# Performance work log

Hardware: AMD Instinct MI355X
Metric: run time of the kernel (lower is better)

The kernel has to match this reference:

```python
import jax, jax.numpy as jnp
import numpy as np

N = 100000   # nodes
E = 3200000  # edges (avg degree 32)
NFEAT = 512
NHID = 8     # forced == 8 by (x_left + x_right) broadcast in the source
NCLASS = 16


def setup_inputs() -> dict:
    key = jax.random.key(0)
    ks = jax.random.split(key, 10)
    x = jax.random.normal(ks[0], (N, NFEAT), dtype=jnp.float32)
    adj_rows = jax.random.randint(ks[1], (E,), 0, N, dtype=jnp.int32)
    adj_cols = jax.random.randint(ks[2], (E,), 0, N, dtype=jnp.int32)
    adj_vals = jax.random.uniform(ks[3], (E,), dtype=jnp.float32)
    s1 = 1.0 / np.sqrt(NFEAT)
    s2 = 1.0 / np.sqrt(NHID)
    W1 = jax.random.normal(ks[4], (NFEAT, NHID), dtype=jnp.float32) * s1
    b1 = jnp.zeros((NHID,), dtype=jnp.float32)
    W2 = jax.random.normal(ks[5], (NHID, NCLASS), dtype=jnp.float32) * s2
    b2 = jnp.zeros((NCLASS,), dtype=jnp.float32)
    V = jax.random.normal(ks[6], (NFEAT, NHID), dtype=jnp.float32) * s1
    gamma = jnp.ones((NHID,), dtype=jnp.float32)
    beta = jnp.zeros((NHID,), dtype=jnp.float32)
    return {"x": x, "adj_rows": adj_rows, "adj_cols": adj_cols, "adj_vals": adj_vals,
            "W1": W1, "b1": b1, "W2": W2, "b2": b2, "V": V, "gamma": gamma, "beta": beta}


def reference(x, adj_rows, adj_cols, adj_vals, W1, b1, W2, b2, V, gamma, beta):
    n = x.shape[0]

    def spmm(support):  # adj @ support, adj in COO
        gathered = adj_vals[:, None] * support[adj_cols]        # [E, F]
        return jax.ops.segment_sum(gathered, adj_rows, num_segments=n)

    # gc1: relu(spmm(adj, x @ W1) + b1)   (dropout off: eval mode)
    x_left = jax.nn.relu(spmm(x @ W1) + b1)                     # [N, 8]

    # BI_Intereaction: FM bi-interaction pooling 0.5*((xV)^2 - (x^2)(V^2))
    xv = x @ V                                                  # [N, 8]
    x2v2 = (x * x) @ (V * V)                                    # [N, 8]
    x_right = jax.nn.relu(0.5 * (xv * xv - x2v2))

    # BatchNorm1d eval mode: running_mean=0, running_var=1 -> affine only
    x_right = gamma * x_right + beta

    h = 0.5 * (x_left + x_right)                                # [N, 8]
    out = spmm(h @ W2) + b2                                     # [N, 16]
    return jax.nn.log_softmax(out, axis=1)
```

## Files before the change

### kernel.cpp

```cpp
#include <hip/hip_runtime.h>
#include <cstdint>
#include <cstddef>


#define NFEAT 512
#define NHID 8
#define NCLASS 16
#define RPB 64
#define NB 512
#define BCAP 2368
#define NBINS_MAX 2048

#define DB_NODES 64
#define DB_CHUNK 32
#define DB_PAD 33
#define DB_BUF (DB_NODES * DB_PAD)

__device__ __forceinline__ void dense_body2(
    int node0, int tid,
    const float* __restrict__ x,
    const float* __restrict__ W1T, const float* __restrict__ VT,
    const float* __restrict__ VSQT,
    const float* __restrict__ gamma, const float* __restrict__ beta,
    float* __restrict__ xw1, float* __restrict__ right, int n_nodes,
    float* xs)
{
    const int lane = tid & 63;

    const int j0 = __builtin_amdgcn_readfirstlane(tid >> 6);
    const float* __restrict__ w1a = W1T  + j0 * NFEAT;
    const float* __restrict__ w1b = W1T  + (j0 + 4) * NFEAT;
    const float* __restrict__ va  = VT   + j0 * NFEAT;
    const float* __restrict__ vb  = VT   + (j0 + 4) * NFEAT;
    const float* __restrict__ sa  = VSQT + j0 * NFEAT;
    const float* __restrict__ sb  = VSQT + (j0 + 4) * NFEAT;

    const int row0 = tid >> 3, row1 = row0 + 32;
    const int col  = tid & 7;
    int gr0 = node0 + row0; if (gr0 >= n_nodes) gr0 = n_nodes - 1;
    int gr1 = node0 + row1; if (gr1 >= n_nodes) gr1 = n_nodes - 1;
    const float4* __restrict__ p0 = (const float4*)(x + (size_t)gr0 * NFEAT) + col;
    const float4* __restrict__ p1 = (const float4*)(x + (size_t)gr1 * NFEAT) + col;
    const int b0 = row0 * DB_PAD + col * 4;
    const int b1 = row1 * DB_PAD + col * 4;

    float a1a = 0.f, a1b = 0.f;
    float ava = 0.f, avb = 0.f;
    float a2a = 0.f, a2b = 0.f;
    const int xbase = lane * DB_PAD;

    {
        float4 c0 = p0[0], c1 = p1[0];
        xs[b0] = c0.x; xs[b0 + 1] = c0.y; xs[b0 + 2] = c0.z; xs[b0 + 3] = c0.w;
        xs[b1] = c1.x; xs[b1 + 1] = c1.y; xs[b1 + 2] = c1.z; xs[b1 + 3] = c1.w;
    }
    __syncthreads();

    for (int ch = 0; ch < NFEAT / DB_CHUNK; ++ch) {
        float4 n0, n1;
        const bool more = (ch + 1) < (NFEAT / DB_CHUNK);
        if (more) { n0 = p0[(ch + 1) * 8]; n1 = p1[(ch + 1) * 8]; }

        const float* xb = xs + (ch & 1) * DB_BUF + xbase;
        const int kof = ch * DB_CHUNK;
#pragma unroll
        for (int kk = 0; kk < DB_CHUNK / 4; ++kk) {
            const int kb = kof + kk * 4;
            float x0 = xb[kk * 4 + 0];
            float x1 = xb[kk * 4 + 1];
            float x2 = xb[kk * 4 + 2];
            float x3 = xb[kk * 4 + 3];
            float q0 = x0 * x0, q1 = x1 * x1, q2 = x2 * x2, q3 = x3 * x3;

            a1a += x0 * w1a[kb] + x1 * w1a[kb + 1] + x2 * w1a[kb + 2] + x3 * w1a[kb + 3];
            a1b += x0 * w1b[kb] + x1 * w1b[kb + 1] + x2 * w1b[kb + 2] + x3 * w1b[kb + 3];
            ava += x0 * va[kb]  + x1 * va[kb + 1]  + x2 * va[kb + 2]  + x3 * va[kb + 3];
            avb += x0 * vb[kb]  + x1 * vb[kb + 1]  + x2 * vb[kb + 2]  + x3 * vb[kb + 3];
            a2a += q0 * sa[kb]  + q1 * sa[kb + 1]  + q2 * sa[kb + 2]  + q3 * sa[kb + 3];
            a2b += q0 * sb[kb]  + q1 * sb[kb + 1]  + q2 * sb[kb + 2]  + q3 * sb[kb + 3];
        }

        if (more) {
            float* d = xs + ((ch + 1) & 1) * DB_BUF;
            d[b0] = n0.x; d[b0 + 1] = n0.y; d[b0 + 2] = n0.z; d[b0 + 3] = n0.w;
            d[b1] = n1.x; d[b1 + 1] = n1.y; d[b1 + 2] = n1.z; d[b1 + 3] = n1.w;
        }
        __syncthreads();
    }

    int node = node0 + lane;
    if (node < n_nodes) {
        float g0 = gamma[j0], g1 = gamma[j0 + 4];
        float b0_ = beta[j0], b1_ = beta[j0 + 4];
        xw1[node * 8 + j0]     = a1a;
        xw1[node * 8 + j0 + 4] = a1b;
        float ra = fmaxf(0.5f * (ava * ava - a2a), 0.f);
        float rb = fmaxf(0.5f * (avb * avb - a2b), 0.f);
        right[node * 8 + j0]     = 0.5f * (g0 * ra + b0_);
        right[node * 8 + j0 + 4] = 0.5f * (g1 * rb + b1_);
    }
}

__global__ __launch_bounds__(256) void dense_kernel(
    const float* __restrict__ x,
    const float* __restrict__ W1T, const float* __restrict__ VT,
    const float* __restrict__ VSQT,
    const float* __restrict__ gamma, const float* __restrict__ beta,
    float* __restrict__ xw1, float* __restrict__ right, int n_nodes)
{
    __shared__ float xs[2 * DB_BUF];
    dense_body2(blockIdx.x * DB_NODES, threadIdx.x, x, W1T, VT, VSQT,
                gamma, beta, xw1, right, n_nodes, xs);
}

__global__ __launch_bounds__(256) void prep_kernel(
    const float* __restrict__ W1, const float* __restrict__ V,
    float* __restrict__ W1T, float* __restrict__ VT, float* __restrict__ VSQT,
    uint4* __restrict__ zero_base, int zero_count16)
{
    int tid = blockIdx.x * 256 + threadIdx.x;
    if (tid < NFEAT * NHID) {
        int k = tid >> 3, j = tid & 7;
        W1T[j * NFEAT + k] = W1[tid];
        float vv = V[tid];
        VT[j * NFEAT + k] = vv;
        VSQT[j * NFEAT + k] = vv * vv;
    }
    int stride = gridDim.x * 256;
    for (int i = tid; i < zero_count16; i += stride)
        zero_base[i] = make_uint4(0u, 0u, 0u, 0u);
}

__global__ __launch_bounds__(256) void count_denseA_kernel(
    const int* __restrict__ rows, int* __restrict__ hist,
    int chunk, int nbins, int e,
    const float* __restrict__ x, const float* __restrict__ W1T,
    const float* __restrict__ VT, const float* __restrict__ VSQT,
    const float* __restrict__ gamma, const float* __restrict__ beta,
    float* __restrict__ xw1, float* __restrict__ right,
    int n_nodes, int dblocksA)
{
    __shared__ float xs[2 * DB_BUF];
    const int bid = blockIdx.x;
    const int tid = threadIdx.x;

    if (bid < dblocksA) {
        dense_body2(bid * DB_NODES, tid, x, W1T, VT, VSQT,
                    gamma, beta, xw1, right, n_nodes, xs);
        return;
    }

    const int cb = bid - dblocksA;
    int* histl = (int*)xs;
    for (int i = tid; i < nbins; i += 256) histl[i] = 0;
    __syncthreads();

    const int base = cb * chunk;
    int lim = e - base; if (lim > chunk) lim = chunk; if (lim < 0) lim = 0;
    const int nq = lim >> 2;
    for (int q = tid; q < nq; q += 256) {
        int4 r4 = *(const int4*)(rows + base + q * 4);
        atomicAdd(&histl[r4.x >> 6], 1);
        atomicAdd(&histl[r4.y >> 6], 1);
        atomicAdd(&histl[r4.z >> 6], 1);
        atomicAdd(&histl[r4.w >> 6], 1);
    }
    const int rem = lim & 3;
    if (tid < rem) atomicAdd(&histl[rows[base + nq * 4 + tid] >> 6], 1);
    __syncthreads();
    for (int i = tid; i < nbins; i += 256)
        hist[(size_t)i * NB + cb] = histl[i];
}

__global__ __launch_bounds__(NB) void scan_kernel(
    const int* __restrict__ hist, int* __restrict__ off,
    int* __restrict__ bintotal)
{
    __shared__ int sa[NB], sb[NB];
    const int bin = blockIdx.x;
    const int tid = threadIdx.x;
    const size_t base = (size_t)bin * NB;

    int h0 = hist[base + tid];
    sa[tid] = h0;
    __syncthreads();
    int* s = sa; int* d = sb;
    for (int o = 1; o < NB; o <<= 1) {
        d[tid] = s[tid] + (tid >= o ? s[tid - o] : 0);
        __syncthreads();
        int* t = s; s = d; d = t;
    }
    off[base + tid] = s[tid] - h0;
    if (tid == NB - 1) bintotal[bin] = s[NB - 1];
}

__global__ __launch_bounds__(256) void place_denseB_kernel(
    const int* __restrict__ rows, const int* __restrict__ cols,
    const float* __restrict__ vals, const int* __restrict__ off,
    unsigned long long* __restrict__ binbuf,
    int chunk, int nbins, int e,
    const float* __restrict__ x, const float* __restrict__ W1T,
    const float* __restrict__ VT, const float* __restrict__ VSQT,
    const float* __restrict__ gamma, const float* __restrict__ beta,
    float* __restrict__ xw1, float* __restrict__ right,
    int n_nodes, int dblocksB, int nodeB0)
{
    __shared__ float xs[2 * DB_BUF];
    const int bid = blockIdx.x;
    const int tid = threadIdx.x;

    if (bid < dblocksB) {
        dense_body2(nodeB0 + bid * DB_NODES, tid, x, W1T, VT, VSQT,
                    gamma, beta, xw1, right, n_nodes, xs);
        return;
    }

    const int cb = bid - dblocksB;
    int* cur = (int*)xs;
    for (int i = tid; i < nbins; i += 256)
        cur[i] = off[(size_t)i * NB + cb];
    __syncthreads();

    const int base = cb * chunk;
    int lim = e - base; if (lim > chunk) lim = chunk; if (lim < 0) lim = 0;
    const int nq = lim >> 2;
    for (int q = tid; q < nq; q += 256) {
        int i = base + q * 4;
        int4   r4 = *(const int4*)(rows + i);
        int4   c4 = *(const int4*)(cols + i);
        float4 v4 = *(const float4*)(vals + i);
#pragma unroll
        for (int u = 0; u < 4; ++u) {
            int r = (&r4.x)[u], c = (&c4.x)[u];
            float v = (&v4.x)[u];
            int bin = r >> 6;
            int slot = atomicAdd(&cur[bin], 1);
            if (slot < BCAP) {
                unsigned long long ev =
                    ((unsigned long long)__float_as_uint(v) << 32) |
                    ((unsigned)(r & (RPB - 1)) << 17) | (unsigned)(unsigned int)c;
                binbuf[(size_t)bin * BCAP + slot] = ev;
            }
        }
    }
    const int rem = lim & 3;
    if (tid < rem) {
        int i = base + nq * 4 + tid;
        int r = rows[i];
        int bin = r >> 6;
        int slot = atomicAdd(&cur[bin], 1);
        if (slot < BCAP) {
            unsigned long long ev =
                ((unsigned long long)__float_as_uint(vals[i]) << 32) |
                ((unsigned)(r & (RPB - 1)) << 17) | (unsigned)(unsigned int)cols[i];
            binbuf[(size_t)bin * BCAP + slot] = ev;
        }
    }
}

__global__ __launch_bounds__(512) void binspmm0_kernel(
    const unsigned long long* __restrict__ binbuf,
    const int* __restrict__ bintotal,
    unsigned long long* __restrict__ sortbuf,
    int* __restrict__ rowstart, int* __restrict__ rowcnt,
    const float* __restrict__ src,
    const float* __restrict__ b1, const float* __restrict__ right,
    float* __restrict__ dst, int n)
{
    __shared__ unsigned long long sorted[BCAP];
    __shared__ int hcnt[RPB];
    __shared__ int hstart[RPB];
    __shared__ int hcur[RPB];
    const int bin = blockIdx.x;
    const int tid = threadIdx.x;

    if (tid < RPB) hcnt[tid] = 0;
    __syncthreads();

    int total = bintotal[bin];
    if (total > BCAP) total = BCAP;
    const unsigned long long* bb = binbuf + (size_t)bin * BCAP;

    const int s0 = tid, s1 = tid + 512, s2 = tid + 1024, s3 = tid + 1536, s4 = tid + 2048;
    unsigned long long e0 = 0, e1 = 0, e2 = 0, e3 = 0, e4 = 0;
    if (s0 < total) { e0 = bb[s0]; atomicAdd(&hcnt[(int)((e0 >> 17) & (RPB - 1))], 1); }
    if (s1 < total) { e1 = bb[s1]; atomicAdd(&hcnt[(int)((e1 >> 17) & (RPB - 1))], 1); }
    if (s2 < total) { e2 = bb[s2]; atomicAdd(&hcnt[(int)((e2 >> 17) & (RPB - 1))], 1); }
    if (s3 < total) { e3 = bb[s3]; atomicAdd(&hcnt[(int)((e3 >> 17) & (RPB - 1))], 1); }
    if (s4 < total) { e4 = bb[s4]; atomicAdd(&hcnt[(int)((e4 >> 17) & (RPB - 1))], 1); }
    __syncthreads();

    if (tid < RPB) hstart[tid] = hcnt[tid];
    __syncthreads();
    for (int o = 1; o < RPB; o <<= 1) {
        int t = 0;
        if (tid < RPB) t = hstart[tid] + (tid >= o ? hstart[tid - o] : 0);
        __syncthreads();
        if (tid < RPB) hstart[tid] = t;
        __syncthreads();
    }
    if (tid < RPB) {
        int ex = hstart[tid] - hcnt[tid];
        hstart[tid] = ex;
        hcur[tid] = ex;
    }
    __syncthreads();

    if (s0 < total) { int rl = (int)((e0 >> 17) & (RPB - 1)); sorted[atomicAdd(&hcur[rl], 1)] = e0; }
    if (s1 < total) { int rl = (int)((e1 >> 17) & (RPB - 1)); sorted[atomicAdd(&hcur[rl], 1)] = e1; }
    if (s2 < total) { int rl = (int)((e2 >> 17) & (RPB - 1)); sorted[atomicAdd(&hcur[rl], 1)] = e2; }
    if (s3 < total) { int rl = (int)((e3 >> 17) & (RPB - 1)); sorted[atomicAdd(&hcur[rl], 1)] = e3; }
    if (s4 < total) { int rl = (int)((e4 >> 17) & (RPB - 1)); sorted[atomicAdd(&hcur[rl], 1)] = e4; }
    __syncthreads();

    for (int s = tid; s < total; s += 512)
        sortbuf[(size_t)bin * BCAP + s] = sorted[s];
    if (tid < RPB) {
        rowstart[bin * RPB + tid] = hstart[tid];
        rowcnt[bin * RPB + tid]   = hcnt[tid];
    }

    const int rl = tid >> 3, l = tid & 7;
    const int st = hstart[rl], cn = hcnt[rl];
    float a0 = 0.f, a1 = 0.f, a2 = 0.f, a3 = 0.f;
    float a4 = 0.f, a5 = 0.f, a6 = 0.f, a7 = 0.f;
    for (int i = st + l; i < st + cn; i += 8) {
        unsigned long long ev = sorted[i];
        int col = (int)(ev & 0x1FFFFu);
        float v = __uint_as_float((unsigned)(ev >> 32));
        const float4* sp = (const float4*)(src + (size_t)col * 8);
        float4 lo = sp[0], hi = sp[1];
        a0 += v * lo.x; a1 += v * lo.y; a2 += v * lo.z; a3 += v * lo.w;
        a4 += v * hi.x; a5 += v * hi.y; a6 += v * hi.z; a7 += v * hi.w;
    }
#pragma unroll
    for (int o2 = 1; o2 < 8; o2 <<= 1) {
        a0 += __shfl_xor(a0, o2); a1 += __shfl_xor(a1, o2);
        a2 += __shfl_xor(a2, o2); a3 += __shfl_xor(a3, o2);
        a4 += __shfl_xor(a4, o2); a5 += __shfl_xor(a5, o2);
        a6 += __shfl_xor(a6, o2); a7 += __shfl_xor(a7, o2);
    }

    const int g = bin * RPB + rl;
    if (g >= n) return;

    float s = l < 4 ? (l < 2 ? (l == 0 ? a0 : a1) : (l == 2 ? a2 : a3))
                    : (l < 6 ? (l == 4 ? a4 : a5) : (l == 6 ? a6 : a7));
    float hv = 0.5f * fmaxf(s + b1[l], 0.f) + right[(size_t)g * 8 + l];
    dst[(size_t)g * 8 + l] = hv;
}

__global__ __launch_bounds__(256) void walk1_kernel(
    const unsigned long long* __restrict__ sortbuf,
    const int* __restrict__ rowstart, const int* __restrict__ rowcnt,
    const float* __restrict__ src,
    const float* __restrict__ W2, const float* __restrict__ b2,
    float* __restrict__ out, int n)
{
    const int bin = blockIdx.x;
    const int tid = threadIdx.x;
    const int rl = tid >> 2, l = tid & 3;

    const int st = rowstart[bin * RPB + rl];
    const int cn = rowcnt[bin * RPB + rl];
    const unsigned long long* bb = sortbuf + (size_t)bin * BCAP;

    float a0 = 0.f, a1 = 0.f, a2 = 0.f, a3 = 0.f;
    float a4 = 0.f, a5 = 0.f, a6 = 0.f, a7 = 0.f;
    for (int i = st + l; i < st + cn; i += 4) {
        unsigned long long ev = bb[i];
        int col = (int)(ev & 0x1FFFFu);
        float v = __uint_as_float((unsigned)(ev >> 32));
        const float4* sp = (const float4*)(src + (size_t)col * 8);
        float4 lo = sp[0], hi = sp[1];
        a0 += v * lo.x; a1 += v * lo.y; a2 += v * lo.z; a3 += v * lo.w;
        a4 += v * hi.x; a5 += v * hi.y; a6 += v * hi.z; a7 += v * hi.w;
    }
#pragma unroll
    for (int o2 = 1; o2 < 4; o2 <<= 1) {
        a0 += __shfl_xor(a0, o2); a1 += __shfl_xor(a1, o2);
        a2 += __shfl_xor(a2, o2); a3 += __shfl_xor(a3, o2);
        a4 += __shfl_xor(a4, o2); a5 += __shfl_xor(a5, o2);
        a6 += __shfl_xor(a6, o2); a7 += __shfl_xor(a7, o2);
    }

    const int g = bin * RPB + rl;
    if (g >= n) return;

    float hv[NHID] = {a0, a1, a2, a3, a4, a5, a6, a7};
    float z[NCLASS];
#pragma unroll
    for (int cc = 0; cc < NCLASS; ++cc) z[cc] = b2[cc];
#pragma unroll
    for (int j = 0; j < NHID; ++j) {
#pragma unroll
        for (int cc = 0; cc < NCLASS; ++cc)
            z[cc] += hv[j] * W2[j * NCLASS + cc];
    }
    float m = z[0];
#pragma unroll
    for (int cc = 1; cc < NCLASS; ++cc) m = fmaxf(m, z[cc]);
    float s = 0.f;
#pragma unroll
    for (int cc = 0; cc < NCLASS; ++cc) s += __expf(z[cc] - m);
    float lse = m + __logf(s);
    float o0, o1, o2, o3;
    if (l == 0)      { o0 = z[0];  o1 = z[1];  o2 = z[2];  o3 = z[3];  }
    else if (l == 1) { o0 = z[4];  o1 = z[5];  o2 = z[6];  o3 = z[7];  }
    else if (l == 2) { o0 = z[8];  o1 = z[9];  o2 = z[10]; o3 = z[11]; }
    else             { o0 = z[12]; o1 = z[13]; o2 = z[14]; o3 = z[15]; }
    *(float4*)(out + (size_t)g * NCLASS + 4 * l) =
        make_float4(o0 - lse, o1 - lse, o2 - lse, o3 - lse);
}

__global__ __launch_bounds__(256) void spmm8_kernel(
    const int* __restrict__ rows, const int* __restrict__ cols,
    const float* __restrict__ vals, const float* __restrict__ src,
    float* __restrict__ acc, int n_edges)
{
    int tid = blockIdx.x * 256 + threadIdx.x;
    int e = tid >> 1;
    if (e >= n_edges) return;
    int hh = tid & 1;
    int r = rows[e], c = cols[e];
    float v = vals[e];
    float4 f = ((const float4*)src)[c * 2 + hh];
    float* d = acc + (size_t)r * NHID + hh * 4;
    unsafeAtomicAdd(d + 0, v * f.x);
    unsafeAtomicAdd(d + 1, v * f.y);
    unsafeAtomicAdd(d + 2, v * f.z);
    unsafeAtomicAdd(d + 3, v * f.w);
}

__global__ __launch_bounds__(256) void mid_kernel(
    const float* __restrict__ acc1, const float* __restrict__ right,
    const float* __restrict__ b1, float* __restrict__ h, int n4)
{
    int i = blockIdx.x * 256 + threadIdx.x;
    if (i >= n4) return;
    float4 a = ((const float4*)acc1)[i];
    float4 r = ((const float4*)right)[i];
    float4 b = ((const float4*)b1)[i & 1];
    float4 o;
    o.x = 0.5f * fmaxf(a.x + b.x, 0.f) + r.x;
    o.y = 0.5f * fmaxf(a.y + b.y, 0.f) + r.y;
    o.z = 0.5f * fmaxf(a.z + b.z, 0.f) + r.z;
    o.w = 0.5f * fmaxf(a.w + b.w, 0.f) + r.w;
    ((float4*)h)[i] = o;
}

__global__ __launch_bounds__(256) void final_kernel(
    const float* __restrict__ acc2, const float* __restrict__ W2,
    const float* __restrict__ b2, float* __restrict__ out, int n_nodes)
{
    int node = blockIdx.x * 256 + threadIdx.x;
    if (node >= n_nodes) return;
    float4 h0 = ((const float4*)acc2)[(size_t)node * 2];
    float4 h1 = ((const float4*)acc2)[(size_t)node * 2 + 1];
    float hv[NHID] = {h0.x, h0.y, h0.z, h0.w, h1.x, h1.y, h1.z, h1.w};
    float z[NCLASS];
#pragma unroll
    for (int c = 0; c < NCLASS; ++c) z[c] = b2[c];
#pragma unroll
    for (int j = 0; j < NHID; ++j) {
#pragma unroll
        for (int c = 0; c < NCLASS; ++c) z[c] += hv[j] * W2[j * NCLASS + c];
    }
    float m = z[0];
#pragma unroll
    for (int c = 1; c < NCLASS; ++c) m = fmaxf(m, z[c]);
    float s = 0.f;
#pragma unroll
    for (int c = 0; c < NCLASS; ++c) s += __expf(z[c] - m);
    float l = m + __logf(s);
    float4* o = (float4*)(out + (size_t)node * NCLASS);
#pragma unroll
    for (int q = 0; q < 4; ++q) {
        float4 tq;
        tq.x = z[4 * q + 0] - l;
        tq.y = z[4 * q + 1] - l;
        tq.z = z[4 * q + 2] - l;
        tq.w = z[4 * q + 3] - l;
        o[q] = tq;
    }
}

extern "C" void kernel_launch(void* const* d_in, const int* in_sizes, int n_in,
                              void* d_out, int out_size, void* d_ws, size_t ws_size,
                              hipStream_t stream)
{
    const float* x     = (const float*)d_in[0];
    const int*   rows  = (const int*)  d_in[1];
    const int*   cols  = (const int*)  d_in[2];
    const float* vals  = (const float*)d_in[3];
    const float* W1    = (const float*)d_in[4];
    const float* b1    = (const float*)d_in[5];
    const float* W2    = (const float*)d_in[6];
    const float* b2    = (const float*)d_in[7];
    const float* V     = (const float*)d_in[8];
    const float* gamma = (const float*)d_in[9];
    const float* beta  = (const float*)d_in[10];

    const int n = in_sizes[0] / NFEAT;
    const int e = in_sizes[1];
    const int nbins = (n + RPB - 1) / RPB;
    const int dblocks = (n + DB_NODES - 1) / DB_NODES;
    const int dblocksA = dblocks / 2;
    const int nodeB0 = dblocksA * DB_NODES;
    const int dblocksB = dblocks - dblocksA;

    float* ws = (float*)d_ws;

    float* xw1   = ws;
    float* right = ws + (size_t)n * 8;
    float* h     = ws + (size_t)n * 16;
    float* W1T   = ws + (size_t)n * 24;
    float* VT    = W1T + NFEAT * NHID;
    float* VSQT  = VT + NFEAT * NHID;
    const size_t fixedf = (size_t)n * 24 + 3 * NFEAT * NHID;
    int* hist     = (int*)(ws + fixedf);
    int* off      = hist + (size_t)nbins * NB;
    int* bintotal = off + (size_t)nbins * NB;
    int* rowstart = bintotal + nbins;
    int* rowcnt   = rowstart + (size_t)nbins * RPB;
    size_t bb_off = (fixedf + 2ull * nbins * NB + nbins + 2ull * nbins * RPB + 1)
                    & ~(size_t)1;
    unsigned long long* binbuf  = (unsigned long long*)(ws + bb_off);
    unsigned long long* sortbuf = binbuf + (size_t)nbins * BCAP;

    const size_t needf = bb_off + 4ull * nbins * BCAP;
    const bool use_fast =
        (n <= (1 << 17)) && (nbins <= NBINS_MAX) && (needf * 4 <= ws_size);

    if (use_fast) {
        int chunk = ((e + NB - 1) / NB + 3) & ~3;

        prep_kernel<<<16, 256, 0, stream>>>(
            W1, V, W1T, VT, VSQT, (uint4*)ws, 0);

        count_denseA_kernel<<<dblocksA + NB, 256, 0, stream>>>(
            rows, hist, chunk, nbins, e,
            x, W1T, VT, VSQT, gamma, beta, xw1, right, n, dblocksA);

        scan_kernel<<<nbins, NB, 0, stream>>>(hist, off, bintotal);

        place_denseB_kernel<<<dblocksB + NB, 256, 0, stream>>>(
            rows, cols, vals, off, binbuf, chunk, nbins, e,
            x, W1T, VT, VSQT, gamma, beta, xw1, right, n, dblocksB, nodeB0);

        binspmm0_kernel<<<nbins, 512, 0, stream>>>(
            binbuf, bintotal, sortbuf, rowstart, rowcnt,
            xw1, b1, right, h, n);

        walk1_kernel<<<nbins, 256, 0, stream>>>(
            sortbuf, rowstart, rowcnt, h, W2, b2, (float*)d_out, n);
    } else {
        float* f_acc1  = ws;
        float* f_acc2  = ws + (size_t)n * 8;
        float* f_xw1   = ws + (size_t)n * 16;
        float* f_right = ws + (size_t)n * 24;
        float* f_h     = ws + (size_t)n * 32;
        float* f_W1T   = ws + (size_t)n * 40;
        float* f_VT    = f_W1T + NFEAT * NHID;
        float* f_VSQT  = f_VT + NFEAT * NHID;

        prep_kernel<<<(n * 4 + 255) / 256, 256, 0, stream>>>(
            W1, V, f_W1T, f_VT, f_VSQT, (uint4*)ws, n * 4);

        dense_kernel<<<dblocks, 256, 0, stream>>>(
            x, f_W1T, f_VT, f_VSQT, gamma, beta, f_xw1, f_right, n);

        spmm8_kernel<<<(e * 2 + 255) / 256, 256, 0, stream>>>(rows, cols, vals, f_xw1, f_acc1, e);
        mid_kernel<<<(n * 2 + 255) / 256, 256, 0, stream>>>(f_acc1, f_right, b1, f_h, n * 2);
        spmm8_kernel<<<(e * 2 + 255) / 256, 256, 0, stream>>>(rows, cols, vals, f_h, f_acc2, e);
        final_kernel<<<(n + 255) / 256, 256, 0, stream>>>(f_acc2, W2, b2, (float*)d_out, n);
    }
}
```

Baseline: 457.0 us.

## Merge prep into count kernel, move all dense work to place, widen gather loops

```diff
diff --git a/kernel.cpp b/kernel.cpp
--- a/kernel.cpp
+++ b/kernel.cpp
@@ -13,7 +13,7 @@
 
 #define DB_NODES 64
 #define DB_CHUNK 32
-#define DB_PAD 33
+#define DB_PAD 36
 #define DB_BUF (DB_NODES * DB_PAD)
 
 __device__ __forceinline__ void dense_body2(
@@ -51,8 +51,8 @@
 
     {
         float4 c0 = p0[0], c1 = p1[0];
-        xs[b0] = c0.x; xs[b0 + 1] = c0.y; xs[b0 + 2] = c0.z; xs[b0 + 3] = c0.w;
-        xs[b1] = c1.x; xs[b1 + 1] = c1.y; xs[b1 + 2] = c1.z; xs[b1 + 3] = c1.w;
+        *(float4*)(xs + b0) = c0;
+        *(float4*)(xs + b1) = c1;
     }
     __syncthreads();
 
@@ -66,10 +66,8 @@
 #pragma unroll
         for (int kk = 0; kk < DB_CHUNK / 4; ++kk) {
             const int kb = kof + kk * 4;
-            float x0 = xb[kk * 4 + 0];
-            float x1 = xb[kk * 4 + 1];
-            float x2 = xb[kk * 4 + 2];
-            float x3 = xb[kk * 4 + 3];
+            float4 xv = *(const float4*)(xb + kk * 4);
+            float x0 = xv.x, x1 = xv.y, x2 = xv.z, x3 = xv.w;
             float q0 = x0 * x0, q1 = x1 * x1, q2 = x2 * x2, q3 = x3 * x3;
 
             a1a += x0 * w1a[kb] + x1 * w1a[kb + 1] + x2 * w1a[kb + 2] + x3 * w1a[kb + 3];
@@ -82,8 +80,8 @@
 
         if (more) {
             float* d = xs + ((ch + 1) & 1) * DB_BUF;
-            d[b0] = n0.x; d[b0 + 1] = n0.y; d[b0 + 2] = n0.z; d[b0 + 3] = n0.w;
-            d[b1] = n1.x; d[b1 + 1] = n1.y; d[b1 + 2] = n1.z; d[b1 + 3] = n1.w;
+            *(float4*)(d + b0) = n0;
+            *(float4*)(d + b1) = n1;
         }
         __syncthreads();
     }
@@ -113,49 +111,29 @@
                 gamma, beta, xw1, right, n_nodes, xs);
 }
 
-__global__ __launch_bounds__(256) void prep_kernel(
+__global__ __launch_bounds__(256) void count_prep_kernel(
+    const int* __restrict__ rows, int* __restrict__ hist,
+    int chunk, int nbins, int e,
     const float* __restrict__ W1, const float* __restrict__ V,
-    float* __restrict__ W1T, float* __restrict__ VT, float* __restrict__ VSQT,
-    uint4* __restrict__ zero_base, int zero_count16)
-{
-    int tid = blockIdx.x * 256 + threadIdx.x;
-    if (tid < NFEAT * NHID) {
-        int k = tid >> 3, j = tid & 7;
-        W1T[j * NFEAT + k] = W1[tid];
-        float vv = V[tid];
+    float* __restrict__ W1T, float* __restrict__ VT, float* __restrict__ VSQT)
+{
+    __shared__ int histl[NBINS_MAX];
+    const int bid = blockIdx.x;
+    const int tid = threadIdx.x;
+
+    int gt = bid * 256 + tid;
+    if (gt < NFEAT * NHID) {
+        int k = gt >> 3, j = gt & 7;
+        W1T[j * NFEAT + k] = W1[gt];
+        float vv = V[gt];
         VT[j * NFEAT + k] = vv;
         VSQT[j * NFEAT + k] = vv * vv;
     }
-    int stride = gridDim.x * 256;
-    for (int i = tid; i < zero_count16; i += stride)
-        zero_base[i] = make_uint4(0u, 0u, 0u, 0u);
-}
-
-__global__ __launch_bounds__(256) void count_denseA_kernel(
-    const int* __restrict__ rows, int* __restrict__ hist,
-    int chunk, int nbins, int e,
-    const float* __restrict__ x, const float* __restrict__ W1T,
-    const float* __restrict__ VT, const float* __restrict__ VSQT,
-    const float* __restrict__ gamma, const float* __restrict__ beta,
-    float* __restrict__ xw1, float* __restrict__ right,
-    int n_nodes, int dblocksA)
-{
-    __shared__ float xs[2 * DB_BUF];
-    const int bid = blockIdx.x;
-    const int tid = threadIdx.x;
-
-    if (bid < dblocksA) {
-        dense_body2(bid * DB_NODES, tid, x, W1T, VT, VSQT,
-                    gamma, beta, xw1, right, n_nodes, xs);
-        return;
-    }
-
-    const int cb = bid - dblocksA;
-    int* histl = (int*)xs;
+
     for (int i = tid; i < nbins; i += 256) histl[i] = 0;
     __syncthreads();
 
-    const int base = cb * chunk;
+    const int base = bid * chunk;
     int lim = e - base; if (lim > chunk) lim = chunk; if (lim < 0) lim = 0;
     const int nq = lim >> 2;
     for (int q = tid; q < nq; q += 256) {
@@ -169,7 +147,7 @@
     if (tid < rem) atomicAdd(&histl[rows[base + nq * 4 + tid] >> 6], 1);
     __syncthreads();
     for (int i = tid; i < nbins; i += 256)
-        hist[(size_t)i * NB + cb] = histl[i];
+        hist[(size_t)i * NB + bid] = histl[i];
 }
 
 __global__ __launch_bounds__(NB) void scan_kernel(
@@ -194,7 +172,7 @@
     if (tid == NB - 1) bintotal[bin] = s[NB - 1];
 }
 
-__global__ __launch_bounds__(256) void place_denseB_kernel(
+__global__ __launch_bounds__(256) void place_dense_kernel(
     const int* __restrict__ rows, const int* __restrict__ cols,
     const float* __restrict__ vals, const int* __restrict__ off,
     unsigned long long* __restrict__ binbuf,
@@ -203,19 +181,19 @@
     const float* __restrict__ VT, const float* __restrict__ VSQT,
     const float* __restrict__ gamma, const float* __restrict__ beta,
     float* __restrict__ xw1, float* __restrict__ right,
-    int n_nodes, int dblocksB, int nodeB0)
+    int n_nodes, int dblocks)
 {
     __shared__ float xs[2 * DB_BUF];
     const int bid = blockIdx.x;
     const int tid = threadIdx.x;
 
-    if (bid < dblocksB) {
-        dense_body2(nodeB0 + bid * DB_NODES, tid, x, W1T, VT, VSQT,
+    if (bid < dblocks) {
+        dense_body2(bid * DB_NODES, tid, x, W1T, VT, VSQT,
                     gamma, beta, xw1, right, n_nodes, xs);
         return;
     }
 
-    const int cb = bid - dblocksB;
+    const int cb = bid - dblocks;
     int* cur = (int*)xs;
     for (int i = tid; i < nbins; i += 256)
         cur[i] = off[(size_t)i * NB + cb];
@@ -321,17 +299,36 @@
     }
 
     const int rl = tid >> 3, l = tid & 7;
-    const int st = hstart[rl], cn = hcnt[rl];
+    const int st = hstart[rl];
+    const int end = st + hcnt[rl];
     float a0 = 0.f, a1 = 0.f, a2 = 0.f, a3 = 0.f;
     float a4 = 0.f, a5 = 0.f, a6 = 0.f, a7 = 0.f;
-    for (int i = st + l; i < st + cn; i += 8) {
-        unsigned long long ev = sorted[i];
-        int col = (int)(ev & 0x1FFFFu);
-        float v = __uint_as_float((unsigned)(ev >> 32));
-        const float4* sp = (const float4*)(src + (size_t)col * 8);
-        float4 lo = sp[0], hi = sp[1];
-        a0 += v * lo.x; a1 += v * lo.y; a2 += v * lo.z; a3 += v * lo.w;
-        a4 += v * hi.x; a5 += v * hi.y; a6 += v * hi.z; a7 += v * hi.w;
+    for (int i = st + l; i < end; i += 32) {
+        const int j1 = i + 8, j2 = i + 16, j3 = i + 24;
+        unsigned long long f0 = sorted[i];
+        unsigned long long f1 = j1 < end ? sorted[j1] : 0ull;
+        unsigned long long f2 = j2 < end ? sorted[j2] : 0ull;
+        unsigned long long f3 = j3 < end ? sorted[j3] : 0ull;
+        int   c0 = (int)(f0 & 0x1FFFFu); float v0 = __uint_as_float((unsigned)(f0 >> 32));
+        int   c1 = (int)(f1 & 0x1FFFFu); float v1 = __uint_as_float((unsigned)(f1 >> 32));
+        int   c2 = (int)(f2 & 0x1FFFFu); float v2 = __uint_as_float((unsigned)(f2 >> 32));
+        int   c3 = (int)(f3 & 0x1FFFFu); float v3 = __uint_as_float((unsigned)(f3 >> 32));
+        const float4* p0 = (const float4*)(src + (size_t)c0 * 8);
+        const float4* p1 = (const float4*)(src + (size_t)c1 * 8);
+        const float4* p2 = (const float4*)(src + (size_t)c2 * 8);
+        const float4* p3 = (const float4*)(src + (size_t)c3 * 8);
+        float4 lo0 = p0[0], hi0 = p0[1];
+        float4 lo1 = p1[0], hi1 = p1[1];
+        float4 lo2 = p2[0], hi2 = p2[1];
+        float4 lo3 = p3[0], hi3 = p3[1];
+        a0 += v0 * lo0.x; a1 += v0 * lo0.y; a2 += v0 * lo0.z; a3 += v0 * lo0.w;
+        a4 += v0 * hi0.x; a5 += v0 * hi0.y; a6 += v0 * hi0.z; a7 += v0 * hi0.w;
+        a0 += v1 * lo1.x; a1 += v1 * lo1.y; a2 += v1 * lo1.z; a3 += v1 * lo1.w;
+        a4 += v1 * hi1.x; a5 += v1 * hi1.y; a6 += v1 * hi1.z; a7 += v1 * hi1.w;
+        a0 += v2 * lo2.x; a1 += v2 * lo2.y; a2 += v2 * lo2.z; a3 += v2 * lo2.w;
+        a4 += v2 * hi2.x; a5 += v2 * hi2.y; a6 += v2 * hi2.z; a7 += v2 * hi2.w;
+        a0 += v3 * lo3.x; a1 += v3 * lo3.y; a2 += v3 * lo3.z; a3 += v3 * lo3.w;
+        a4 += v3 * hi3.x; a5 += v3 * hi3.y; a6 += v3 * hi3.z; a7 += v3 * hi3.w;
     }
 #pragma unroll
     for (int o2 = 1; o2 < 8; o2 <<= 1) {
@@ -350,7 +347,7 @@
     dst[(size_t)g * 8 + l] = hv;
 }
 
-__global__ __launch_bounds__(256) void walk1_kernel(
+__global__ __launch_bounds__(512) void walk1_kernel(
     const unsigned long long* __restrict__ sortbuf,
     const int* __restrict__ rowstart, const int* __restrict__ rowcnt,
     const float* __restrict__ src,
@@ -359,25 +356,43 @@
 {
     const int bin = blockIdx.x;
     const int tid = threadIdx.x;
-    const int rl = tid >> 2, l = tid & 3;
+    const int rl = tid >> 3, l = tid & 7;
 
     const int st = rowstart[bin * RPB + rl];
-    const int cn = rowcnt[bin * RPB + rl];
+    const int end = st + rowcnt[bin * RPB + rl];
     const unsigned long long* bb = sortbuf + (size_t)bin * BCAP;
 
     float a0 = 0.f, a1 = 0.f, a2 = 0.f, a3 = 0.f;
     float a4 = 0.f, a5 = 0.f, a6 = 0.f, a7 = 0.f;
-    for (int i = st + l; i < st + cn; i += 4) {
-        unsigned long long ev = bb[i];
-        int col = (int)(ev & 0x1FFFFu);
-        float v = __uint_as_float((unsigned)(ev >> 32));
-        const float4* sp = (const float4*)(src + (size_t)col * 8);
-        float4 lo = sp[0], hi = sp[1];
-        a0 += v * lo.x; a1 += v * lo.y; a2 += v * lo.z; a3 += v * lo.w;
-        a4 += v * hi.x; a5 += v * hi.y; a6 += v * hi.z; a7 += v * hi.w;
-    }
-#pragma unroll
-    for (int o2 = 1; o2 < 4; o2 <<= 1) {
+    for (int i = st + l; i < end; i += 32) {
+        const int j1 = i + 8, j2 = i + 16, j3 = i + 24;
+        unsigned long long f0 = bb[i];
+        unsigned long long f1 = j1 < end ? bb[j1] : 0ull;
+        unsigned long long f2 = j2 < end ? bb[j2] : 0ull;
+        unsigned long long f3 = j3 < end ? bb[j3] : 0ull;
+        int   c0 = (int)(f0 & 0x1FFFFu); float v0 = __uint_as_float((unsigned)(f0 >> 32));
+        int   c1 = (int)(f1 & 0x1FFFFu); float v1 = __uint_as_float((unsigned)(f1 >> 32));
+        int   c2 = (int)(f2 & 0x1FFFFu); float v2 = __uint_as_float((unsigned)(f2 >> 32));
+        int   c3 = (int)(f3 & 0x1FFFFu); float v3 = __uint_as_float((unsigned)(f3 >> 32));
+        const float4* p0 = (const float4*)(src + (size_t)c0 * 8);
+        const float4* p1 = (const float4*)(src + (size_t)c1 * 8);
+        const float4* p2 = (const float4*)(src + (size_t)c2 * 8);
+        const float4* p3 = (const float4*)(src + (size_t)c3 * 8);
+        float4 lo0 = p0[0], hi0 = p0[1];
+        float4 lo1 = p1[0], hi1 = p1[1];
+        float4 lo2 = p2[0], hi2 = p2[1];
+        float4 lo3 = p3[0], hi3 = p3[1];
+        a0 += v0 * lo0.x; a1 += v0 * lo0.y; a2 += v0 * lo0.z; a3 += v0 * lo0.w;
+        a4 += v0 * hi0.x; a5 += v0 * hi0.y; a6 += v0 * hi0.z; a7 += v0 * hi0.w;
+        a0 += v1 * lo1.x; a1 += v1 * lo1.y; a2 += v1 * lo1.z; a3 += v1 * lo1.w;
+        a4 += v1 * hi1.x; a5 += v1 * hi1.y; a6 += v1 * hi1.z; a7 += v1 * hi1.w;
+        a0 += v2 * lo2.x; a1 += v2 * lo2.y; a2 += v2 * lo2.z; a3 += v2 * lo2.w;
+        a4 += v2 * hi2.x; a5 += v2 * hi2.y; a6 += v2 * hi2.z; a7 += v2 * hi2.w;
+        a0 += v3 * lo3.x; a1 += v3 * lo3.y; a2 += v3 * lo3.z; a3 += v3 * lo3.w;
+        a4 += v3 * hi3.x; a5 += v3 * hi3.y; a6 += v3 * hi3.z; a7 += v3 * hi3.w;
+    }
+#pragma unroll
+    for (int o2 = 1; o2 < 8; o2 <<= 1) {
         a0 += __shfl_xor(a0, o2); a1 += __shfl_xor(a1, o2);
         a2 += __shfl_xor(a2, o2); a3 += __shfl_xor(a3, o2);
         a4 += __shfl_xor(a4, o2); a5 += __shfl_xor(a5, o2);
@@ -388,29 +403,39 @@
     if (g >= n) return;
 
     float hv[NHID] = {a0, a1, a2, a3, a4, a5, a6, a7};
-    float z[NCLASS];
-#pragma unroll
-    for (int cc = 0; cc < NCLASS; ++cc) z[cc] = b2[cc];
+    float z0 = b2[2 * l], z1 = b2[2 * l + 1];
 #pragma unroll
     for (int j = 0; j < NHID; ++j) {
-#pragma unroll
-        for (int cc = 0; cc < NCLASS; ++cc)
-            z[cc] += hv[j] * W2[j * NCLASS + cc];
-    }
-    float m = z[0];
-#pragma unroll
-    for (int cc = 1; cc < NCLASS; ++cc) m = fmaxf(m, z[cc]);
-    float s = 0.f;
-#pragma unroll
-    for (int cc = 0; cc < NCLASS; ++cc) s += __expf(z[cc] - m);
+        float2 w = *(const float2*)(W2 + j * NCLASS + 2 * l);
+        z0 += hv[j] * w.x;
+        z1 += hv[j] * w.y;
+    }
+    float m = fmaxf(z0, z1);
+#pragma unroll
+    for (int o2 = 1; o2 < 8; o2 <<= 1) m = fmaxf(m, __shfl_xor(m, o2));
+    float s = __expf(z0 - m) + __expf(z1 - m);
+#pragma unroll
+    for (int o2 = 1; o2 < 8; o2 <<= 1) s += __shfl_xor(s, o2);
     float lse = m + __logf(s);
-    float o0, o1, o2, o3;
-    if (l == 0)      { o0 = z[0];  o1 = z[1];  o2 = z[2];  o3 = z[3];  }
-    else if (l == 1) { o0 = z[4];  o1 = z[5];  o2 = z[6];  o3 = z[7];  }
-    else if (l == 2) { o0 = z[8];  o1 = z[9];  o2 = z[10]; o3 = z[11]; }
-    else             { o0 = z[12]; o1 = z[13]; o2 = z[14]; o3 = z[15]; }
-    *(float4*)(out + (size_t)g * NCLASS + 4 * l) =
-        make_float4(o0 - lse, o1 - lse, o2 - lse, o3 - lse);
+    *(float2*)(out + (size_t)g * NCLASS + 2 * l) = make_float2(z0 - lse, z1 - lse);
+}
+
+__global__ __launch_bounds__(256) void prep_kernel(
+    const float* __restrict__ W1, const float* __restrict__ V,
+    float* __restrict__ W1T, float* __restrict__ VT, float* __restrict__ VSQT,
+    uint4* __restrict__ zero_base, int zero_count16)
+{
+    int tid = blockIdx.x * 256 + threadIdx.x;
+    if (tid < NFEAT * NHID) {
+        int k = tid >> 3, j = tid & 7;
+        W1T[j * NFEAT + k] = W1[tid];
+        float vv = V[tid];
+        VT[j * NFEAT + k] = vv;
+        VSQT[j * NFEAT + k] = vv * vv;
+    }
+    int stride = gridDim.x * 256;
+    for (int i = tid; i < zero_count16; i += stride)
+        zero_base[i] = make_uint4(0u, 0u, 0u, 0u);
 }
 
 __global__ __launch_bounds__(256) void spmm8_kernel(
@@ -505,9 +530,6 @@
     const int e = in_sizes[1];
     const int nbins = (n + RPB - 1) / RPB;
     const int dblocks = (n + DB_NODES - 1) / DB_NODES;
-    const int dblocksA = dblocks / 2;
-    const int nodeB0 = dblocksA * DB_NODES;
-    const int dblocksB = dblocks - dblocksA;
 
     float* ws = (float*)d_ws;
 
@@ -535,24 +557,20 @@
     if (use_fast) {
         int chunk = ((e + NB - 1) / NB + 3) & ~3;
 
-        prep_kernel<<<16, 256, 0, stream>>>(
-            W1, V, W1T, VT, VSQT, (uint4*)ws, 0);
-
-        count_denseA_kernel<<<dblocksA + NB, 256, 0, stream>>>(
-            rows, hist, chunk, nbins, e,
-            x, W1T, VT, VSQT, gamma, beta, xw1, right, n, dblocksA);
+        count_prep_kernel<<<NB, 256, 0, stream>>>(
+            rows, hist, chunk, nbins, e, W1, V, W1T, VT, VSQT);
 
         scan_kernel<<<nbins, NB, 0, stream>>>(hist, off, bintotal);
 
-        place_denseB_kernel<<<dblocksB + NB, 256, 0, stream>>>(
+        place_dense_kernel<<<dblocks + NB, 256, 0, stream>>>(
             rows, cols, vals, off, binbuf, chunk, nbins, e,
-            x, W1T, VT, VSQT, gamma, beta, xw1, right, n, dblocksB, nodeB0);
+            x, W1T, VT, VSQT, gamma, beta, xw1, right, n, dblocks);
 
         binspmm0_kernel<<<nbins, 512, 0, stream>>>(
             binbuf, bintotal, sortbuf, rowstart, rowcnt,
             xw1, b1, right, h, n);
 
-        walk1_kernel<<<nbins, 256, 0, stream>>>(
+        walk1_kernel<<<nbins, 512, 0, stream>>>(
             sortbuf, rowstart, rowcnt, h, W2, b2, (float*)d_out, n);
     } else {
         float* f_acc1  = ws;
```

After: 452.2 us. Within noise of the previous version (-1.0%).
